# Performance work log

Hardware: AMD Instinct MI355X
Metric: run time of the kernel (lower is better)

Reference implementation:

```python
import jax, jax.numpy as jnp
import numpy as np

L = 3
NUM_KERNELS = 16
BATCH = 128   # conv in/out channels (torch 'batch_size')
SLIDE = 256   # slide_len, acts as conv batch dim
D = 128       # embedding width, equals conv kernel width


def setup_inputs() -> dict:
    key = jax.random.key(0)
    ks = jax.random.split(key, 7)
    # number of kernels per height h=1,2,3 for idx % 3 pattern over 16 kernels
    counts = [len(range(h, NUM_KERNELS, L)) for h in range(L)]  # [6, 5, 5]
    inp = {
        "Ec": jax.random.normal(ks[0], (BATCH, SLIDE, L, D), dtype=jnp.float32),
        "W1": jax.random.normal(ks[1], (counts[0], BATCH, BATCH, 1, D), dtype=jnp.float32) * 0.05,
        "W2": jax.random.normal(ks[2], (counts[1], BATCH, BATCH, 2, D), dtype=jnp.float32) * 0.05,
        "W3": jax.random.normal(ks[3], (counts[2], BATCH, BATCH, 3, D), dtype=jnp.float32) * 0.05,
        "b1": jax.random.normal(ks[4], (counts[0], BATCH), dtype=jnp.float32) * 0.05,
        "b2": jax.random.normal(ks[5], (counts[1], BATCH), dtype=jnp.float32) * 0.05,
        "b3": jax.random.normal(ks[6], (counts[2], BATCH), dtype=jnp.float32) * 0.05,
    }
    return inp


def reference(Ec, W1, W2, W3, b1, b2, b3):
    # Ec: (B, S, L, d) -> transpose to (S, B, L, d); S is the conv batch dim,
    # B is the channel dim (Conv2d(batch_size, batch_size, (h, d))).
    Ec_t = jnp.transpose(Ec, (1, 0, 2, 3))  # (S, B, L, d)
    Ws = [W1, W2, W3]
    bs = [b1, b2, b3]
    res = [None] * NUM_KERNELS  # each entry: (S, B)
    for h_idx in range(L):
        h = h_idx + 1
        P = L - h + 1  # conv output height == maxpool window
        idxs = list(range(h_idx, NUM_KERNELS, L))  # kernels with this height
        # windows: (P, S, B, h, d) -- the P valid vertical positions
        windows = jnp.stack([Ec_t[:, :, p:p + h, :] for p in range(P)], axis=0)
        # conv over (channel, h, d): (P, k, S, out_channel=B)
        conv = jnp.einsum('pscad,kocad->pkso', windows, Ws[h_idx])
        conv = conv + bs[h_idx][None, :, None, :]
        # maxpool over the P positions, then ReLU
        pooled = jax.nn.relu(jnp.max(conv, axis=0))  # (k, S, B)
        for j, idx in enumerate(idxs):
            res[idx] = pooled[j]
    out = jnp.stack(res, axis=-1)  # (S, B, K)
    # torch: (S,B,K,1) -> transpose(0,1) -> transpose(-1,-2) => (B, S, 1, K)
    return jnp.transpose(out, (1, 0, 2))[:, :, None, :]
```

## Files before the change

kernel.cpp:

```cpp
#include <hip/hip_runtime.h>
#include <hip/hip_bf16.h>

#define NBATCH 128
#define NSLIDE 256
#define PART_ELEMS 32768
#define NPART 424

using ushort4v = __attribute__((ext_vector_type(4))) unsigned short;
using bf16x8   = __attribute__((ext_vector_type(8))) __bf16;
using floatx4  = __attribute__((ext_vector_type(4))) float;

__device__ __forceinline__ unsigned short f2bf(float f) {
  union { float f; unsigned u; } v; v.f = f;
  unsigned r = v.u + 0x7fffu + ((v.u >> 16) & 1u);
  return (unsigned short)(r >> 16);
}

__device__ __forceinline__ ushort4v pack4(const float4& a) {
  unsigned lo, hi;
  asm("v_cvt_pk_bf16_f32 %0, %1, %2" : "=v"(lo) : "v"(a.x), "v"(a.y));
  asm("v_cvt_pk_bf16_f32 %0, %1, %2" : "=v"(hi) : "v"(a.z), "v"(a.w));
  union { unsigned u[2]; ushort4v v; } r;
  r.u[0] = lo; r.u[1] = hi;
  return r.v;
}

__global__ __launch_bounds__(256, 3) void gemm_uniform(
    const float* __restrict__ Ec,
    const float* __restrict__ W1, const float* __restrict__ W2,
    const float* __restrict__ W3,
    unsigned short* __restrict__ part)
{
  const int bx = blockIdx.x;
  const int ch = bx & 7;
  const int i  = bx >> 3;
  int htype, k, a, p, m;
  if (i < 36) {
    htype = 0; k = i / 6; int mem = i - k * 6;
    a = 0; p = mem >> 1; m = mem & 1;
  } else if (i < 76) {
    htype = 1; int t = i - 36; int g = t >> 2, mem = t & 3;
    k = g >> 1; a = g & 1; p = mem >> 1; m = mem & 1;
  } else {
    htype = 2; int t = i - 76; int g = t >> 1;
    k = g / 3; a = g - k * 3; p = 0; m = t & 1;
  }
  const int l = p + a;
  const int h = htype + 1;
  const float* wbase = (htype == 0) ? W1 : ((htype == 1) ? W2 : W3);
  const long o_stride = 16384L * h;
  const long c_stride = 128L * h;

  int slot, seq;
  if (htype == 0)      { slot = 3 * k + p;      seq = ch; }
  else if (htype == 1) { slot = 18 + 2 * k + p; seq = a * 8 + ch; }
  else                 { slot = 28 + k;         seq = a * 8 + ch; }
  int pbase;
  if (slot < 18)      pbase = slot * 8;
  else if (slot < 28) pbase = 144 + (slot - 18) * 16;
  else                pbase = 304 + (slot - 28) * 24;
  const int pslot = pbase + seq;

  __shared__ __align__(16) unsigned short As[128 * 64];
  __shared__ __align__(16) unsigned short Bs[128 * 64];

  const int tid = threadIdx.x;
  const int c16 = tid & 15;
  const int r0  = tid >> 4;
  const int gh   = c16 >> 1;
  const int half4 = (c16 & 1) * 4;

  const float* aP = Ec + (long)l * 128 + (long)(m * 128 + r0) * 384 + c16 * 4;
  const float* wP = wbase + (long)k * 128 * o_stride + (long)a * 128
                    + (long)r0 * o_stride + c16 * 4;

  const int wave = tid >> 6;
  const int lane = tid & 63;
  const int wm = (wave >> 1) * 64;
  const int wn = (wave & 1) * 64;
  const int lr = lane & 15;
  const int lq = lane >> 4;

  floatx4 acc[4][4];
#pragma unroll
  for (int i2 = 0; i2 < 4; ++i2)
#pragma unroll
    for (int j = 0; j < 4; ++j) acc[i2][j] = (floatx4){0.f, 0.f, 0.f, 0.f};

  float4 aL[8], wL[8];

#define LOAD_TILE(t_)                                                           \
  {                                                                             \
    const int tv = (t_);                                                        \
    const long cA = (long)(ch * 16 + (tv >> 1)) * 98304 + (long)(tv & 1) * 64;  \
    const long cB = (long)(ch * 16 + (tv >> 1)) * c_stride + (long)(tv & 1) * 64;\
    _Pragma("unroll")                                                           \
    for (int q = 0; q < 8; ++q) {                                               \
      aL[q] = *reinterpret_cast<const float4*>(aP + cA + (long)q * (16 * 384)); \
      wL[q] = *reinterpret_cast<const float4*>(wP + cB + (long)q * 16 * o_stride);\
    }                                                                           \
  }

  LOAD_TILE(0);

  for (int t = 0; t < 32; ++t) {
#pragma unroll
    for (int q = 0; q < 8; ++q) {
      const int row = r0 + 16 * q;
      const int off = row * 64 + ((gh ^ (row & 7)) << 3) + half4;
      *reinterpret_cast<ushort4v*>(&As[off]) = pack4(aL[q]);
      *reinterpret_cast<ushort4v*>(&Bs[off]) = pack4(wL[q]);
    }
    if (t + 1 < 32) LOAD_TILE(t + 1);
    __syncthreads();

#pragma unroll
    for (int ks = 0; ks < 2; ++ks) {
      bf16x8 af[4], bf_[4];
#pragma unroll
      for (int i2 = 0; i2 < 4; ++i2) {
        const int row = wm + 16 * i2 + lr;
        const int col = (((ks * 4 + lq) ^ (row & 7)) << 3);
        af[i2] = *reinterpret_cast<const bf16x8*>(&As[row * 64 + col]);
      }
#pragma unroll
      for (int j = 0; j < 4; ++j) {
        const int row = wn + 16 * j + lr;
        const int col = (((ks * 4 + lq) ^ (row & 7)) << 3);
        bf_[j] = *reinterpret_cast<const bf16x8*>(&Bs[row * 64 + col]);
      }
#pragma unroll
      for (int i2 = 0; i2 < 4; ++i2)
#pragma unroll
        for (int j = 0; j < 4; ++j)
          acc[i2][j] = __builtin_amdgcn_mfma_f32_16x16x32_bf16(af[i2], bf_[j], acc[i2][j], 0, 0, 0);
    }
    __syncthreads();
  }
#undef LOAD_TILE

  unsigned short* base = part + (long)pslot * PART_ELEMS + (long)m * 128 * NBATCH;
#pragma unroll
  for (int i2 = 0; i2 < 4; ++i2) {
#pragma unroll
    for (int j = 0; j < 4; ++j) {
#pragma unroll
      for (int r = 0; r < 4; ++r) {
        int s = wm + 16 * i2 + lq * 4 + r;
        int o = wn + 16 * j + lr;
        base[s * NBATCH + o] = f2bf(acc[i2][j][r]);
      }
    }
  }
}

__device__ __forceinline__ float bf2f(unsigned short u) {
  union { unsigned u; float f; } v; v.u = ((unsigned)u) << 16; return v.f;
}

__global__ void epilogue(const unsigned short* __restrict__ part,
                         const float* __restrict__ b1, const float* __restrict__ b2,
                         const float* __restrict__ b3, float* __restrict__ out)
{
  int t = blockIdx.x * 256 + threadIdx.x;
  int o = t & 127;
  int s = t >> 7;
  const long idx = (long)s * NBATCH + o;

  float v[33];
#pragma unroll
  for (int sl = 0; sl < 18; ++sl) {
    float a = 0.f;
#pragma unroll
    for (int c = 0; c < 8; ++c) a += bf2f(part[(long)(sl * 8 + c) * PART_ELEMS + idx]);
    v[sl] = a;
  }
#pragma unroll
  for (int sl = 0; sl < 10; ++sl) {
    float a = 0.f;
#pragma unroll
    for (int c = 0; c < 16; ++c) a += bf2f(part[(long)(144 + sl * 16 + c) * PART_ELEMS + idx]);
    v[18 + sl] = a;
  }
#pragma unroll
  for (int sl = 0; sl < 5; ++sl) {
    float a = 0.f;
#pragma unroll
    for (int c = 0; c < 24; ++c) a += bf2f(part[(long)(304 + sl * 24 + c) * PART_ELEMS + idx]);
    v[28 + sl] = a;
  }

  float r[16];
#pragma unroll
  for (int k = 0; k < 6; ++k) {
    float mx = fmaxf(fmaxf(v[3 * k + 0], v[3 * k + 1]), v[3 * k + 2]);
    r[3 * k + 0] = fmaxf(mx + b1[k * 128 + o], 0.f);
  }
#pragma unroll
  for (int k = 0; k < 5; ++k) {
    float mx = fmaxf(v[18 + 2 * k], v[18 + 2 * k + 1]);
    r[3 * k + 1] = fmaxf(mx + b2[k * 128 + o], 0.f);
  }
#pragma unroll
  for (int k = 0; k < 5; ++k) {
    r[3 * k + 2] = fmaxf(v[28 + k] + b3[k * 128 + o], 0.f);
  }
  float* op = out + ((long)o * 256 + s) * 16;
  reinterpret_cast<float4*>(op)[0] = make_float4(r[0], r[1], r[2], r[3]);
  reinterpret_cast<float4*>(op)[1] = make_float4(r[4], r[5], r[6], r[7]);
  reinterpret_cast<float4*>(op)[2] = make_float4(r[8], r[9], r[10], r[11]);
  reinterpret_cast<float4*>(op)[3] = make_float4(r[12], r[13], r[14], r[15]);
}

extern "C" void kernel_launch(void* const* d_in, const int* in_sizes, int n_in,
                              void* d_out, int out_size, void* d_ws, size_t ws_size,
                              hipStream_t stream) {
  const float* Ec = (const float*)d_in[0];
  const float* W1 = (const float*)d_in[1];
  const float* W2 = (const float*)d_in[2];
  const float* W3 = (const float*)d_in[3];
  const float* b1 = (const float*)d_in[4];
  const float* b2 = (const float*)d_in[5];
  const float* b3 = (const float*)d_in[6];
  float* out = (float*)d_out;
  unsigned short* part = (unsigned short*)d_ws;

  gemm_uniform<<<848, 256, 0, stream>>>(Ec, W1, W2, W3, part);
  epilogue<<<(NSLIDE * NBATCH) / 256, 256, 0, stream>>>(part, b1, b2, b3, out);
}
```

Measured before the change: 385.8 us.

## Double-buffer LDS tiles in GEMM and split epilogue into parallel reduce plus finalize

The GEMM kernel now uses two shared-memory buffers, so the next tile is stored while the current one feeds the MFMAs, and it drops from one barrier pair per tile to a single barrier. Launch bounds go from 3 to 2 blocks per CU to make room for the doubled LDS. The old epilogue, which ran only 128 blocks doing strided scalar reads of the partials, is replaced by a reduce kernel over 528 blocks with vectorised 8-wide bf16 loads and fp32 sums written to workspace, followed by a small finalize kernel. This adds a third launch and an extra fp32 round-trip through memory.

```diff
diff --git a/kernel.cpp b/kernel.cpp
--- a/kernel.cpp
+++ b/kernel.cpp
@@ -5,8 +5,10 @@
 #define NSLIDE 256
 #define PART_ELEMS 32768
 #define NPART 424
+#define SUMS_OFF_SHORTS (NPART * PART_ELEMS)
 
 using ushort4v = __attribute__((ext_vector_type(4))) unsigned short;
+using ushort8v = __attribute__((ext_vector_type(8))) unsigned short;
 using bf16x8   = __attribute__((ext_vector_type(8))) __bf16;
 using floatx4  = __attribute__((ext_vector_type(4))) float;
 
@@ -25,7 +27,11 @@
   return r.v;
 }
 
-__global__ __launch_bounds__(256, 3) void gemm_uniform(
+__device__ __forceinline__ float bf2f(unsigned short u) {
+  union { unsigned u; float f; } v; v.u = ((unsigned)u) << 16; return v.f;
+}
+
+__global__ __launch_bounds__(256, 2) void gemm_uniform(
     const float* __restrict__ Ec,
     const float* __restrict__ W1, const float* __restrict__ W2,
     const float* __restrict__ W3,
@@ -61,8 +67,8 @@
   else                pbase = 304 + (slot - 28) * 24;
   const int pslot = pbase + seq;
 
-  __shared__ __align__(16) unsigned short As[128 * 64];
-  __shared__ __align__(16) unsigned short Bs[128 * 64];
+  __shared__ __align__(16) unsigned short As[2][128 * 64];
+  __shared__ __align__(16) unsigned short Bs[2][128 * 64];
 
   const int tid = threadIdx.x;
   const int c16 = tid & 15;
@@ -101,19 +107,24 @@
     }                                                                           \
   }
 
+#define STORE_TILE(b_)                                                          \
+  {                                                                             \
+    _Pragma("unroll")                                                           \
+    for (int q = 0; q < 8; ++q) {                                               \
+      const int row = r0 + 16 * q;                                              \
+      const int off = row * 64 + ((gh ^ (row & 7)) << 3) + half4;               \
+      *reinterpret_cast<ushort4v*>(&As[b_][off]) = pack4(aL[q]);                \
+      *reinterpret_cast<ushort4v*>(&Bs[b_][off]) = pack4(wL[q]);                \
+    }                                                                           \
+  }
+
   LOAD_TILE(0);
-
+  STORE_TILE(0);
+  LOAD_TILE(1);
+  __syncthreads();
+
+  int cur = 0;
   for (int t = 0; t < 32; ++t) {
-#pragma unroll
-    for (int q = 0; q < 8; ++q) {
-      const int row = r0 + 16 * q;
-      const int off = row * 64 + ((gh ^ (row & 7)) << 3) + half4;
-      *reinterpret_cast<ushort4v*>(&As[off]) = pack4(aL[q]);
-      *reinterpret_cast<ushort4v*>(&Bs[off]) = pack4(wL[q]);
-    }
-    if (t + 1 < 32) LOAD_TILE(t + 1);
-    __syncthreads();
-
 #pragma unroll
     for (int ks = 0; ks < 2; ++ks) {
       bf16x8 af[4], bf_[4];
@@ -121,13 +132,13 @@
       for (int i2 = 0; i2 < 4; ++i2) {
         const int row = wm + 16 * i2 + lr;
         const int col = (((ks * 4 + lq) ^ (row & 7)) << 3);
-        af[i2] = *reinterpret_cast<const bf16x8*>(&As[row * 64 + col]);
+        af[i2] = *reinterpret_cast<const bf16x8*>(&As[cur][row * 64 + col]);
       }
 #pragma unroll
       for (int j = 0; j < 4; ++j) {
         const int row = wn + 16 * j + lr;
         const int col = (((ks * 4 + lq) ^ (row & 7)) << 3);
-        bf_[j] = *reinterpret_cast<const bf16x8*>(&Bs[row * 64 + col]);
+        bf_[j] = *reinterpret_cast<const bf16x8*>(&Bs[cur][row * 64 + col]);
       }
 #pragma unroll
       for (int i2 = 0; i2 < 4; ++i2)
@@ -135,9 +146,15 @@
         for (int j = 0; j < 4; ++j)
           acc[i2][j] = __builtin_amdgcn_mfma_f32_16x16x32_bf16(af[i2], bf_[j], acc[i2][j], 0, 0, 0);
     }
+    if (t < 31) {
+      STORE_TILE(cur ^ 1);
+      if (t < 30) LOAD_TILE(t + 2);
+    }
     __syncthreads();
+    cur ^= 1;
   }
 #undef LOAD_TILE
+#undef STORE_TILE
 
   unsigned short* base = part + (long)pslot * PART_ELEMS + (long)m * 128 * NBATCH;
 #pragma unroll
@@ -154,41 +171,59 @@
   }
 }
 
-__device__ __forceinline__ float bf2f(unsigned short u) {
-  union { unsigned u; float f; } v; v.u = ((unsigned)u) << 16; return v.f;
-}
-
-__global__ void epilogue(const unsigned short* __restrict__ part,
+__global__ void reduce_part(const unsigned short* __restrict__ part,
+                            float* __restrict__ sums)
+{
+  const int t = blockIdx.x * 256 + threadIdx.x;
+  const int sl   = t >> 12;
+  const int col8 = t & 4095;
+
+  int cb, cc;
+  if (sl < 18)      { cb = sl * 8;             cc = 8;  }
+  else if (sl < 28) { cb = 144 + (sl - 18) * 16; cc = 16; }
+  else              { cb = 304 + (sl - 28) * 24; cc = 24; }
+
+  const unsigned short* p0 = part + (long)cb * PART_ELEMS + (long)col8 * 8;
+
+  float acc[8];
+#pragma unroll
+  for (int j = 0; j < 8; ++j) acc[j] = 0.f;
+
+#define ADD8(c_)                                                        \
+  {                                                                     \
+    ushort8v v = *reinterpret_cast<const ushort8v*>(p0 + (long)(c_) * PART_ELEMS); \
+    _Pragma("unroll")                                                   \
+    for (int j = 0; j < 8; ++j) acc[j] += bf2f(v[j]);                   \
+  }
+
+#pragma unroll
+  for (int c = 0; c < 8; ++c) ADD8(c);
+  if (cc > 8) {
+#pragma unroll
+    for (int c = 8; c < 16; ++c) ADD8(c);
+  }
+  if (cc > 16) {
+#pragma unroll
+    for (int c = 16; c < 24; ++c) ADD8(c);
+  }
+#undef ADD8
+
+  float* sp = sums + (long)sl * PART_ELEMS + (long)col8 * 8;
+  reinterpret_cast<float4*>(sp)[0] = make_float4(acc[0], acc[1], acc[2], acc[3]);
+  reinterpret_cast<float4*>(sp)[1] = make_float4(acc[4], acc[5], acc[6], acc[7]);
+}
+
+__global__ void finalize(const float* __restrict__ sums,
                          const float* __restrict__ b1, const float* __restrict__ b2,
                          const float* __restrict__ b3, float* __restrict__ out)
 {
-  int t = blockIdx.x * 256 + threadIdx.x;
-  int o = t & 127;
-  int s = t >> 7;
-  const long idx = (long)s * NBATCH + o;
+  const int t = blockIdx.x * 256 + threadIdx.x;
+  const int o = t & 127;
+  const int s = t >> 7;
 
   float v[33];
 #pragma unroll
-  for (int sl = 0; sl < 18; ++sl) {
-    float a = 0.f;
-#pragma unroll
-    for (int c = 0; c < 8; ++c) a += bf2f(part[(long)(sl * 8 + c) * PART_ELEMS + idx]);
-    v[sl] = a;
-  }
-#pragma unroll
-  for (int sl = 0; sl < 10; ++sl) {
-    float a = 0.f;
-#pragma unroll
-    for (int c = 0; c < 16; ++c) a += bf2f(part[(long)(144 + sl * 16 + c) * PART_ELEMS + idx]);
-    v[18 + sl] = a;
-  }
-#pragma unroll
-  for (int sl = 0; sl < 5; ++sl) {
-    float a = 0.f;
-#pragma unroll
-    for (int c = 0; c < 24; ++c) a += bf2f(part[(long)(304 + sl * 24 + c) * PART_ELEMS + idx]);
-    v[28 + sl] = a;
-  }
+  for (int sl = 0; sl < 33; ++sl) v[sl] = sums[(long)sl * PART_ELEMS + t];
 
   float r[16];
 #pragma unroll
@@ -224,7 +259,9 @@
   const float* b3 = (const float*)d_in[6];
   float* out = (float*)d_out;
   unsigned short* part = (unsigned short*)d_ws;
+  float* sums = (float*)((unsigned short*)d_ws + SUMS_OFF_SHORTS);
 
   gemm_uniform<<<848, 256, 0, stream>>>(Ec, W1, W2, W3, part);
-  epilogue<<<(NSLIDE * NBATCH) / 256, 256, 0, stream>>>(part, b1, b2, b3, out);
-}
+  reduce_part<<<(33 * 4096) / 256, 256, 0, stream>>>(part, sums);
+  finalize<<<(NSLIDE * NBATCH) / 256, 256, 0, stream>>>(sums, b1, b2, b3, out);
+}
```

Measured after the change: 376.0 us. 2.5% less time.
